# Kernel optimization log

Hardware: AMD Instinct MI355X
Metric: run time of the kernel (lower is better)

## Reference

```python
import jax, jax.numpy as jnp
import numpy as np

IOU_THRESHOLDS = (0.5, 0.75)
B, N, G = 256, 4000, 50


def _iou(amin, amax, bmin, bmax):
    # broadcasted temporal IoU: anchors [N,1] vs boxes [1,G] -> [N,G]
    inter = jnp.maximum(jnp.minimum(amax, bmax) - jnp.maximum(amin, bmin), 0.0)
    union = (amax - amin) + (bmax - bmin) - inter
    return inter / union


def _greedy_tp(segments, gts, thr):
    # segments: [N,2], gts: [G,2]. Replicates AP.get_values greedy matching:
    # for each label (in order), claim the first (lowest-index) unused proposal
    # whose IoU > thr. Final used-mask == is_TP.
    ious = _iou(segments[:, 0:1], segments[:, 1:2], gts[None, :, 0], gts[None, :, 1])  # [N,G]
    pot = ious > thr
    n = segments.shape[0]

    def step(used, col):  # col: [N] bool, candidates for this label
        cand = col & ~used
        idx = jnp.argmax(cand)  # first True (argmax of bool is first max)
        used = jnp.where(jnp.any(cand), used.at[idx].set(True), used)
        return used, None

    used, _ = jax.lax.scan(step, jnp.zeros((n,), jnp.bool_), pot.T)
    return used  # [N] bool


def _ap_for_threshold(scores, segments, labels, thr):
    is_tp = jax.vmap(lambda s, g: _greedy_tp(s, g, thr))(segments, labels)  # [B,N]
    conf = scores.reshape(-1)                       # [B*N]
    tp = is_tp.reshape(-1).astype(jnp.float32)
    order = jnp.argsort(-conf)                      # sort by confidence, descending
    tp = tp[order]
    n_labels = labels.shape[0] * labels.shape[1]
    m = tp.shape[0]
    acc_tp = jnp.cumsum(tp)
    precision = acc_tp / (jnp.arange(m, dtype=jnp.float32) + 1.0)
    recall = acc_tp / jnp.float32(n_labels)
    # curve = [[1,0]] then (recall, precision) reversed; AP = sum(|dx| * cummax(y)[:-1])
    x = jnp.concatenate([jnp.ones((1,), jnp.float32), recall[::-1]])
    y = jnp.concatenate([jnp.zeros((1,), jnp.float32), precision[::-1]])
    y_max = jax.lax.cummax(y, axis=0)
    x_diff = jnp.abs(jnp.diff(x))
    return jnp.sum(x_diff * y_max[:-1])


def setup_inputs() -> dict:
    key = jax.random.key(0)
    k1, k2, k3, k4, k5 = jax.random.split(key, 5)
    scores = jax.random.uniform(k1, (B, N), dtype=jnp.float32)
    p_start = jax.random.uniform(k2, (B, N), dtype=jnp.float32) * 0.9
    p_len = jax.random.uniform(k3, (B, N), dtype=jnp.float32) * 0.1 + 0.005
    segments = jnp.stack([p_start, p_start + p_len], axis=-1)  # [B,N,2], start<end
    g_start = jax.random.uniform(k4, (B, G), dtype=jnp.float32) * 0.9
    g_len = jax.random.uniform(k5, (B, G), dtype=jnp.float32) * 0.1 + 0.005
    labels = jnp.stack([g_start, g_start + g_len], axis=-1)    # [B,G,2]
    return {"scores": scores, "segments": segments, "labels": labels}


def reference(scores, segments, labels):
    # returns AP at each IoU threshold, shape [len(IOU_THRESHOLDS)]
    return jnp.stack([_ap_for_threshold(scores, segments, labels, t) for t in IOU_THRESHOLDS])
```

## Files before the change

### kernel.cpp

```cpp
#include <hip/hip_runtime.h>


#define B_ 256
#define N_ 4000
#define G_ 50
#define M_ (B_ * N_)
#define NL_ (B_ * G_)
#define NBKT 4096
#define SBKT 2048

typedef unsigned long long u64;

__device__ __forceinline__ unsigned bucket_of(float c) {
    unsigned b = (unsigned)(c * 4096.0f);
    return b > (NBKT - 1) ? (NBKT - 1) : b;
}

__global__ __launch_bounds__(1024) void tp_kernel(
    const float* __restrict__ seg,
    const float* __restrict__ gts,
    const float* __restrict__ conf,
    int* __restrict__ tpIdx,
    int* __restrict__ cnt,
    unsigned short* __restrict__ pbh)
{
    const int tid  = threadIdx.x;
    const int lane = tid & 63;
    const int wv   = tid >> 6;
    const int b    = blockIdx.x;

    __shared__ float2 gtl[G_];
    __shared__ u64 cand[2][G_][64];
    __shared__ unsigned hls[NBKT / 2];
    __shared__ int lcnt[2];

    #pragma unroll
    for (int k = 0; k < NBKT / 2048; ++k) hls[k * 1024 + tid] = 0u;
    if (tid < G_) gtl[tid] = ((const float2*)gts)[b * G_ + tid];
    if (tid < 2) lcnt[tid] = 0;
    __syncthreads();

    const float* cb = conf + (size_t)b * N_;
    #pragma unroll
    for (int s = 0; s < 4; ++s) {
        int n = s * 1024 + tid;
        if (n < N_) {
            unsigned bin = bucket_of(cb[n]);
            atomicAdd(&hls[bin >> 1], 1u << ((bin & 1) * 16));
        }
    }

    const float2* sb = (const float2*)(seg + (size_t)b * (N_ * 2));
    float pmin[4], pmax[4], plen[4];
    #pragma unroll
    for (int s = 0; s < 4; ++s) {
        int n = s * 1024 + tid;
        if (n < N_) { float2 v = sb[n]; pmin[s] = v.x; pmax[s] = v.y; }
        else { pmin[s] = 1e9f; pmax[s] = 1e9f; }
        plen[s] = pmax[s] - pmin[s];
    }
    for (int g = 0; g < G_; ++g) {
        float2 gt = gtl[g];
        float glen = gt.y - gt.x;
        u64 m0[4], m1[4];
        #pragma unroll
        for (int s = 0; s < 4; ++s) {
            float inter = fmaxf(fminf(pmax[s], gt.y) - fmaxf(pmin[s], gt.x), 0.0f);
            float uni = plen[s] + glen - inter;
            float e25 = uni * 0x1p-25f;
            float d   = inter - 0.5f * uni;
            m0[s] = __ballot(d > e25);
            m1[s] = __ballot((d - 0.25f * uni) > e25);
        }
        if (lane == 0) {
            #pragma unroll
            for (int s = 0; s < 4; ++s) {
                cand[0][g][s * 16 + wv] = m0[s];
                cand[1][g][s * 16 + wv] = m1[s];
            }
        }
    }
    __syncthreads();

    {
        unsigned* prow = (unsigned*)(pbh + (size_t)b * NBKT);
        #pragma unroll
        for (int k = 0; k < NBKT / 2048; ++k)
            prow[k * 1024 + tid] = hls[k * 1024 + tid];
    }

    if (wv < 2) {
        const int thr_i = wv;
        u64 used = 0ull;
        for (int g = 0; g < G_; ++g) {
            u64 c = cand[thr_i][g][lane] & ~used;
            u64 ball = __ballot(c != 0ull);
            if (ball) {
                int fl = __ffsll(ball) - 1;
                if (lane == fl) used |= (c & (0ull - c));
            }
        }
        int cpop = __popcll(used);
        if (cpop) {
            int j = atomicAdd(&lcnt[thr_i], cpop);
            u64 u = used;
            while (u) {
                int bit = __ffsll(u) - 1;
                u &= u - 1;
                tpIdx[thr_i * NL_ + b * G_ + j++] = b * N_ + lane * 64 + bit;
            }
        }
    }
    __syncthreads();
    if (tid < 2) cnt[tid * B_ + b] = lcnt[tid];
}

__global__ __launch_bounds__(256) void s1_kernel(
    unsigned short* __restrict__ pbh,
    unsigned* __restrict__ total)
{
    __shared__ unsigned short tile[256][32];
    const int j = blockIdx.x;
    const int t = threadIdx.x;
    uint4* dst = (uint4*)&tile[t][0];
    const uint4* src = (const uint4*)(pbh + (size_t)t * NBKT + j * 32);
    #pragma unroll
    for (int k = 0; k < 4; ++k) dst[k] = src[k];
    __syncthreads();
    if (t < 32) {
        unsigned run = 0;
        for (int b = 0; b < 256; ++b) {
            unsigned v = tile[b][t];
            tile[b][t] = (unsigned short)run;
            run += v;
        }
        total[j * 32 + t] = run;
    }
    __syncthreads();
    uint4* back = (uint4*)(pbh + (size_t)t * NBKT + j * 32);
    #pragma unroll
    for (int k = 0; k < 4; ++k) back[k] = dst[k];
}

__global__ __launch_bounds__(1024) void scatter_kernel(
    const float* __restrict__ conf,
    const unsigned short* __restrict__ pbh,
    const unsigned* __restrict__ total,
    unsigned* __restrict__ binStartG,
    u64* __restrict__ sKey)
{
    __shared__ unsigned baseB[NBKT];
    __shared__ unsigned lofs[NBKT];
    const int tid = threadIdx.x;
    const int b = blockIdx.x;

    unsigned* part = lofs;
    uint4 v4 = ((const uint4*)total)[tid];
    unsigned s = v4.x + v4.y + v4.z + v4.w;
    part[tid] = s;
    __syncthreads();
    for (int off = 1; off < 1024; off <<= 1) {
        unsigned add = (tid >= off) ? part[tid - off] : 0u;
        __syncthreads();
        part[tid] += add;
        __syncthreads();
    }
    unsigned base = (tid == 0) ? 0u : part[tid - 1];
    __syncthreads();
    baseB[4 * tid]     = base;
    baseB[4 * tid + 1] = base + v4.x;
    baseB[4 * tid + 2] = base + v4.x + v4.y;
    baseB[4 * tid + 3] = base + v4.x + v4.y + v4.z;
    __syncthreads();
    #pragma unroll
    for (int k = 0; k < 4; ++k) {
        int bin = k * 1024 + tid;
        unsigned bs = baseB[bin];
        if (b == 0) binStartG[bin] = bs;
        baseB[bin] = bs + pbh[(size_t)b * NBKT + bin];
        lofs[bin] = 0u;
    }
    __syncthreads();

    const float* cb = conf + (size_t)b * N_;
    #pragma unroll
    for (int s4 = 0; s4 < 4; ++s4) {
        int n = s4 * 1024 + tid;
        if (n < N_) {
            float c = cb[n];
            unsigned bin = bucket_of(c);
            unsigned lo = atomicAdd(&lofs[bin], 1u);
            unsigned idx = (unsigned)(b * N_ + n);
            sKey[baseB[bin] + lo] = ((u64)__float_as_uint(c) << 32) | (u64)(0xFFFFFFFFu - idx);
        }
    }
}

__global__ __launch_bounds__(256) void rank_kernel(
    const float* __restrict__ conf,
    const int* __restrict__ tpIdx,
    const int* __restrict__ cnt,
    const unsigned* __restrict__ total,
    const unsigned* __restrict__ binStart,
    const u64* __restrict__ sKey,
    int* __restrict__ tpRank)
{
    const int lane = threadIdx.x & 63;
    const int w = (blockIdx.x << 2) | (threadIdx.x >> 6);
    if (w >= 2 * NL_) return;
    const int thr_i = w / NL_;
    const int t = w - thr_i * NL_;
    const int batch = t / G_;
    const int j = t - batch * G_;

    if (j < cnt[thr_i * B_ + batch]) {
        int e = tpIdx[thr_i * NL_ + t];
        float c = conf[e];
        u64 keyE = ((u64)__float_as_uint(c) << 32) | (u64)(0xFFFFFFFFu - (unsigned)e);
        unsigned bin = bucket_of(c);
        unsigned lo = binStart[bin], n = total[bin];
        int r = M_ - (int)lo - (int)n;
        for (unsigned base = 0; base < n; base += 64) {
            unsigned k = base + lane;
            bool pred = (k < n) && (sKey[lo + k] > keyE);
            r += (int)__popcll(__ballot(pred));
        }
        if (lane == 0) tpRank[thr_i * NL_ + t] = r;
    } else {
        if (lane == 0) tpRank[thr_i * NL_ + t] = M_ + t;
    }
}

__global__ __launch_bounds__(1024) void sortap_kernel(
    const int* __restrict__ tpRank,
    float* __restrict__ out)
{
    const int C = 13;
    union U1 { unsigned part[1024]; float cmax[1024]; };
    union U2 { unsigned hist[SBKT]; double red[1024]; };
    __shared__ int sr[NL_];
    __shared__ U1 u1;
    __shared__ U2 u2;
    const int thr_i = blockIdx.x;
    const int t = threadIdx.x;

    u2.hist[t] = 0u; u2.hist[t + 1024] = 0u;
    __syncthreads();

    int r[C]; unsigned beta[C];
    #pragma unroll
    for (int k = 0; k < C; ++k) {
        int i = t + k * 1024;
        if (i < NL_) {
            int rr = tpRank[thr_i * NL_ + i];
            r[k] = rr;
            unsigned bb = ((unsigned)rr) >> 9;
            beta[k] = bb > (SBKT - 1) ? (SBKT - 1) : bb;
            atomicAdd(&u2.hist[beta[k]], 1u);
        } else { r[k] = 0; beta[k] = 0xFFFFFFFFu; }
    }
    __syncthreads();

    unsigned h0 = u2.hist[2 * t], h1 = u2.hist[2 * t + 1];
    u1.part[t] = h0 + h1;
    __syncthreads();
    for (int off = 1; off < 1024; off <<= 1) {
        unsigned add = (t >= off) ? u1.part[t - off] : 0u;
        __syncthreads();
        u1.part[t] += add;
        __syncthreads();
    }
    unsigned base = (t == 0) ? 0u : u1.part[t - 1];
    __syncthreads();
    u2.hist[2 * t] = base;
    u2.hist[2 * t + 1] = base + h0;
    __syncthreads();

    #pragma unroll
    for (int k = 0; k < C; ++k)
        if (beta[k] != 0xFFFFFFFFu) {
            unsigned slot = atomicAdd(&u2.hist[beta[k]], 1u);
            sr[slot] = r[k];
        }
    __syncthreads();

    int p[C];
    #pragma unroll
    for (int k = 0; k < C; ++k) {
        if (beta[k] != 0xFFFFFFFFu) {
            unsigned st = (beta[k] == 0u) ? 0u : u2.hist[beta[k] - 1];
            unsigned en = u2.hist[beta[k]];
            int c = 0;
            for (unsigned j = st; j < en; ++j) c += (sr[j] < r[k]);
            p[k] = (int)st + c;
        } else p[k] = -1;
    }
    __syncthreads();
    #pragma unroll
    for (int k = 0; k < C; ++k)
        if (p[k] >= 0) sr[p[k]] = r[k];
    __syncthreads();

    float pr[C]; int rk[C];
    #pragma unroll
    for (int k = 0; k < C; ++k) {
        int i = t * C + k;
        rk[k] = (i < NL_) ? sr[i] : 0x7FFFFFFF;
        pr[k] = (rk[k] < M_) ? (float)(i + 1) / (float)(rk[k] + 1) : -1.0f;
    }
    float suf[C];
    float run = -1.0f;
    #pragma unroll
    for (int k = C - 1; k >= 0; --k) { run = fmaxf(run, pr[k]); suf[k] = run; }

    u1.cmax[t] = run;
    __syncthreads();
    for (int off = 1; off < 1024; off <<= 1) {
        float v = u1.cmax[t];
        float o = (t + off < 1024) ? u1.cmax[t + off] : -1.0f;
        __syncthreads();
        u1.cmax[t] = fmaxf(v, o);
        __syncthreads();
    }
    float follow = (t + 1 < 1024) ? u1.cmax[t + 1] : -1.0f;

    double acc = 0.0;
    #pragma unroll
    for (int k = 0; k < C; ++k) {
        int i = t * C + k;
        if (rk[k] >= 1 && rk[k] < M_) {
            float smax = fmaxf(suf[k], follow);
            float rhi = (float)(i + 1) / 12800.0f;
            float rlo = (float)i / 12800.0f;
            acc += (double)((rhi - rlo) * smax);
        }
    }
    __syncthreads();
    u2.red[t] = acc;
    __syncthreads();
    for (int off = 512; off >= 1; off >>= 1) {
        if (t < off) u2.red[t] += u2.red[t + off];
        __syncthreads();
    }
    if (t == 0) out[thr_i] = (float)u2.red[0];
}

extern "C" void kernel_launch(void* const* d_in, const int* in_sizes, int n_in,
                              void* d_out, int out_size, void* d_ws, size_t ws_size,
                              hipStream_t stream) {
    const float* scores = (const float*)d_in[0];
    const float* seg    = (const float*)d_in[1];
    const float* gts    = (const float*)d_in[2];
    float* out = (float*)d_out;

    char* p = (char*)d_ws;
    int*            cnt        = (int*)p;             p += 4096;
    int*            tpIdx      = (int*)p;             p += 2 * NL_ * 4;
    int*            tpRank     = (int*)p;             p += 2 * NL_ * 4;
    unsigned*       total      = (unsigned*)p;        p += NBKT * 4;
    unsigned*       binStart   = (unsigned*)p;        p += NBKT * 4;
    unsigned short* pbh        = (unsigned short*)p;  p += (size_t)B_ * NBKT * 2;
    u64*            sKey       = (u64*)p;             p += (size_t)M_ * 8;
    (void)ws_size; (void)in_sizes; (void)n_in; (void)out_size;

    tp_kernel<<<B_, 1024, 0, stream>>>(seg, gts, scores, tpIdx, cnt, pbh);
    s1_kernel<<<NBKT / 32, 256, 0, stream>>>(pbh, total);
    scatter_kernel<<<B_, 1024, 0, stream>>>(scores, pbh, total, binStart, sKey);
    rank_kernel<<<(2 * NL_ + 3) / 4, 256, 0, stream>>>(scores, tpIdx, cnt,
                                                       total, binStart, sKey, tpRank);
    sortap_kernel<<<2, 1024, 0, stream>>>(tpRank, out);
}
```

Measured before the change: 163.8 us.

## Replace barrier-heavy shared-memory scans with wavefront shuffle scans

The block-wide Hillis-Steele scans in the scatter and sortap kernels, each needing two barriers per step, become two-level scans: a shuffle within each 64-lane wavefront, then a scan over the per-wave totals. The serial 256-step column prefix sum in s1_kernel, which used only 32 threads, is split across 8 segments per column with a segment-offset pass. The goal is to cut barrier count and serial latency in these small kernels, at the cost of slightly more complex index logic.

```diff
diff --git a/kernel.cpp b/kernel.cpp
--- a/kernel.cpp
+++ b/kernel.cpp
@@ -120,6 +120,7 @@
     unsigned* __restrict__ total)
 {
     __shared__ unsigned short tile[256][32];
+    __shared__ unsigned segsum[8][32];
     const int j = blockIdx.x;
     const int t = threadIdx.x;
     uint4* dst = (uint4*)&tile[t][0];
@@ -127,14 +128,23 @@
     #pragma unroll
     for (int k = 0; k < 4; ++k) dst[k] = src[k];
     __syncthreads();
-    if (t < 32) {
-        unsigned run = 0;
-        for (int b = 0; b < 256; ++b) {
-            unsigned v = tile[b][t];
-            tile[b][t] = (unsigned short)run;
-            run += v;
-        }
-        total[j * 32 + t] = run;
+
+    const int col = t & 31, seg = t >> 5;
+    unsigned run = 0;
+    #pragma unroll
+    for (int i = 0; i < 32; ++i) run += tile[seg * 32 + i][col];
+    segsum[seg][col] = run;
+    __syncthreads();
+    unsigned off0 = 0;
+    #pragma unroll
+    for (int s = 0; s < 8; ++s) off0 += (s < seg) ? segsum[s][col] : 0u;
+    if (seg == 7) total[j * 32 + col] = off0 + segsum[7][col];
+    unsigned run2 = off0;
+    #pragma unroll
+    for (int i = 0; i < 32; ++i) {
+        unsigned v = tile[seg * 32 + i][col];
+        tile[seg * 32 + i][col] = (unsigned short)run2;
+        run2 += v;
     }
     __syncthreads();
     uint4* back = (uint4*)(pbh + (size_t)t * NBKT + j * 32);
@@ -151,26 +161,38 @@
 {
     __shared__ unsigned baseB[NBKT];
     __shared__ unsigned lofs[NBKT];
+    __shared__ unsigned wtot[16];
     const int tid = threadIdx.x;
+    const int lane = tid & 63;
+    const int wv = tid >> 6;
     const int b = blockIdx.x;
 
-    unsigned* part = lofs;
     uint4 v4 = ((const uint4*)total)[tid];
-    unsigned s = v4.x + v4.y + v4.z + v4.w;
-    part[tid] = s;
-    __syncthreads();
-    for (int off = 1; off < 1024; off <<= 1) {
-        unsigned add = (tid >= off) ? part[tid - off] : 0u;
-        __syncthreads();
-        part[tid] += add;
-        __syncthreads();
-    }
-    unsigned base = (tid == 0) ? 0u : part[tid - 1];
-    __syncthreads();
-    baseB[4 * tid]     = base;
-    baseB[4 * tid + 1] = base + v4.x;
-    baseB[4 * tid + 2] = base + v4.x + v4.y;
-    baseB[4 * tid + 3] = base + v4.x + v4.y + v4.z;
+    unsigned own = v4.x + v4.y + v4.z + v4.w;
+    unsigned inc = own;
+    #pragma unroll
+    for (int off = 1; off < 64; off <<= 1) {
+        unsigned o = __shfl_up(inc, off, 64);
+        if (lane >= off) inc += o;
+    }
+    if (lane == 63) wtot[wv] = inc;
+    __syncthreads();
+    if (wv == 0) {
+        unsigned w = (lane < 16) ? wtot[lane] : 0u;
+        unsigned wi = w;
+        #pragma unroll
+        for (int off = 1; off < 16; off <<= 1) {
+            unsigned o = __shfl_up(wi, off, 64);
+            if (lane >= off) wi += o;
+        }
+        if (lane < 16) wtot[lane] = wi - w;
+    }
+    __syncthreads();
+    unsigned start = (inc - own) + wtot[wv];
+    baseB[4 * tid]     = start;
+    baseB[4 * tid + 1] = start + v4.x;
+    baseB[4 * tid + 2] = start + v4.x + v4.y;
+    baseB[4 * tid + 3] = start + v4.x + v4.y + v4.z;
     __syncthreads();
     #pragma unroll
     for (int k = 0; k < 4; ++k) {
@@ -236,13 +258,15 @@
     float* __restrict__ out)
 {
     const int C = 13;
-    union U1 { unsigned part[1024]; float cmax[1024]; };
+    union U1 { unsigned wtot[16]; float wmaxs[16]; };
     union U2 { unsigned hist[SBKT]; double red[1024]; };
     __shared__ int sr[NL_];
     __shared__ U1 u1;
     __shared__ U2 u2;
     const int thr_i = blockIdx.x;
     const int t = threadIdx.x;
+    const int lane = t & 63;
+    const int wv = t >> 6;
 
     u2.hist[t] = 0u; u2.hist[t + 1024] = 0u;
     __syncthreads();
@@ -262,15 +286,27 @@
     __syncthreads();
 
     unsigned h0 = u2.hist[2 * t], h1 = u2.hist[2 * t + 1];
-    u1.part[t] = h0 + h1;
-    __syncthreads();
-    for (int off = 1; off < 1024; off <<= 1) {
-        unsigned add = (t >= off) ? u1.part[t - off] : 0u;
-        __syncthreads();
-        u1.part[t] += add;
-        __syncthreads();
-    }
-    unsigned base = (t == 0) ? 0u : u1.part[t - 1];
+    unsigned own = h0 + h1;
+    unsigned inc = own;
+    #pragma unroll
+    for (int off = 1; off < 64; off <<= 1) {
+        unsigned o = __shfl_up(inc, off, 64);
+        if (lane >= off) inc += o;
+    }
+    if (lane == 63) u1.wtot[wv] = inc;
+    __syncthreads();
+    if (wv == 0) {
+        unsigned w = (lane < 16) ? u1.wtot[lane] : 0u;
+        unsigned wi = w;
+        #pragma unroll
+        for (int off = 1; off < 16; off <<= 1) {
+            unsigned o = __shfl_up(wi, off, 64);
+            if (lane >= off) wi += o;
+        }
+        if (lane < 16) u1.wtot[lane] = wi - w;
+    }
+    __syncthreads();
+    unsigned base = (inc - own) + u1.wtot[wv];
     __syncthreads();
     u2.hist[2 * t] = base;
     u2.hist[2 * t + 1] = base + h0;
@@ -313,16 +349,30 @@
     #pragma unroll
     for (int k = C - 1; k >= 0; --k) { run = fmaxf(run, pr[k]); suf[k] = run; }
 
-    u1.cmax[t] = run;
-    __syncthreads();
-    for (int off = 1; off < 1024; off <<= 1) {
-        float v = u1.cmax[t];
-        float o = (t + off < 1024) ? u1.cmax[t + off] : -1.0f;
-        __syncthreads();
-        u1.cmax[t] = fmaxf(v, o);
-        __syncthreads();
-    }
-    float follow = (t + 1 < 1024) ? u1.cmax[t + 1] : -1.0f;
+    float m = run;
+    #pragma unroll
+    for (int off = 1; off < 64; off <<= 1) {
+        float o = __shfl_down(m, off, 64);
+        if (lane + off < 64) m = fmaxf(m, o);
+    }
+    float f_in = __shfl_down(m, 1, 64);
+    if (lane == 63) f_in = -1.0f;
+    if (lane == 0) u1.wmaxs[wv] = m;
+    __syncthreads();
+    if (wv == 0) {
+        float wm = (lane < 16) ? u1.wmaxs[lane] : -1.0f;
+        float mi = wm;
+        #pragma unroll
+        for (int off = 1; off < 16; off <<= 1) {
+            float o = __shfl_down(mi, off, 64);
+            if (lane + off < 64) mi = fmaxf(mi, o);
+        }
+        float fw = __shfl_down(mi, 1, 64);
+        if (lane >= 15) fw = -1.0f;
+        if (lane < 16) u1.wmaxs[lane] = fw;
+    }
+    __syncthreads();
+    float follow = fmaxf(f_in, u1.wmaxs[wv]);
 
     double acc = 0.0;
     #pragma unroll
```

Measured after the change: 159.0 us. -2.9%, faster.
